# Performance work log

Hardware: AMD Instinct MI355X
Metric: run time of the kernel (lower is better)

## Reference

```python
import jax, jax.numpy as jnp
import numpy as np
import math

B, L, M, D, EL, H = 128, 105, 55, 256, 3, 1
PATCH = [3, 5, 7]

def pos_embed(T, d):
    pos = jnp.arange(T, dtype=jnp.float32)[:, None]
    div = jnp.exp(jnp.arange(0, d, 2, dtype=jnp.float32) * (-math.log(10000.0) / d))
    pe = jnp.zeros((T, d), dtype=jnp.float32)
    pe = pe.at[:, 0::2].set(jnp.sin(pos * div))
    pe = pe.at[:, 1::2].set(jnp.cos(pos * div))
    return pe

def circular_conv(x, w):
    # x: [N, T, Cin], w: [Dout, Cin, 3]; Conv1d kernel 3, circular padding 1, no bias
    xc = jnp.pad(x.transpose(0, 2, 1), ((0, 0), (0, 0), (1, 1)), mode='wrap')
    y = jax.lax.conv_general_dilated(xc, w, (1,), 'VALID', dimension_numbers=('NCH', 'OIH', 'NCH'))
    return y.transpose(0, 2, 1)

def _forward(x, conv_p0, conv_n0, conv_p1, conv_n1, conv_p2, conv_n2, Wq, bq, Wk, bk):
    convs = [(conv_p0, conv_n0), (conv_p1, conv_n1), (conv_p2, conv_n2)]
    # RevIN 'norm': per-sample standardization over time; stats are detached in torch
    mean = jax.lax.stop_gradient(jnp.mean(x, axis=1, keepdims=True))
    std = jax.lax.stop_gradient(jnp.sqrt(jnp.var(x, axis=1, keepdims=True) + 1e-5))
    xr = (x - mean) / std                      # [B, L, M]
    xt = xr.transpose(0, 2, 1)                 # [B, M, L]
    dk = D // H
    scale = 1.0 / math.sqrt(dk)
    series_list, prior_list = [], []
    for i, p in enumerate(PATCH):
        n = L // p
        # patch-size branch: (b m) n p -> embed over n with in_channels=p
        x_size = circular_conv(xt.reshape(B * M, n, p), convs[i][0]) + pos_embed(n, D)
        # patch-num branch: (b m) p n -> embed over p with in_channels=n
        x_num = circular_conv(xt.reshape(B * M, p, n), convs[i][1]) + pos_embed(p, D)
        for l in range(EL):
            def attn_mean(z):
                T = z.shape[1]
                q = (z @ Wq[l] + bq[l]).reshape(B * M, T, H, dk)
                k = (z @ Wk[l] + bk[l]).reshape(B * M, T, H, dk)
                a = jax.nn.softmax(scale * jnp.einsum('blhe,bshe->bhls', q, k), axis=-1)
                # fuse: mean over channel BEFORE expanding to window size
                # (repeat/tile commutes with the channel-mean, avoids [B*M,H,L,L])
                return a.reshape(B, M, H, T, T).mean(axis=1)   # [B, H, T, T]
            a_size = attn_mean(x_size)                          # [B, H, n, n]
            # einops repeat '(m rm) (n rn)': element-wise contiguous repeat
            series_list.append(jnp.repeat(jnp.repeat(a_size, p, axis=-2), p, axis=-1))
            a_num = attn_mean(x_num)                            # [B, H, p, p]
            # torch .repeat: tiling
            prior_list.append(jnp.tile(a_num, (1, 1, n, n)))
    # order: patch-major, layer-minor (matches the flattened lists)
    return jnp.stack(series_list), jnp.stack(prior_list)        # each [9, B, H, L, L]

def setup_inputs():
    key = jax.random.key(0)
    ks = jax.random.split(key, 12)
    s = 0.05
    inp = {"x": jax.random.normal(ks[0], (B, L, M), jnp.float32)}
    for i, p in enumerate(PATCH):
        inp[f"conv_p{i}"] = s * jax.random.normal(ks[1 + 2 * i], (D, p, 3), jnp.float32)
        inp[f"conv_n{i}"] = s * jax.random.normal(ks[2 + 2 * i], (D, L // p, 3), jnp.float32)
    inp["Wq"] = s * jax.random.normal(ks[7], (EL, D, D), jnp.float32)
    inp["bq"] = jnp.zeros((EL, D), jnp.float32)
    inp["Wk"] = s * jax.random.normal(ks[8], (EL, D, D), jnp.float32)
    inp["bk"] = jnp.zeros((EL, D), jnp.float32)
    return inp

def reference(x, conv_p0, conv_n0, conv_p1, conv_n1, conv_p2, conv_n2, Wq, bq, Wk, bk):
    return _forward(x, conv_p0, conv_n0, conv_p1, conv_n1, conv_p2, conv_n2, Wq, bq, Wk, bk)
```

## Files before the change

### kernel.cpp

```cpp
#include <hip/hip_runtime.h>
#include <hip/hip_bf16.h>

#define B_ 128
#define L_ 105
#define M_ 55
#define D_ 256
#define NCOMBO 18

#define WS_XT    0
#define WS_PE    739200
#define WS_LEFT  761216
#define WS_RIGHT 1258880
#define WS_MM    1756544
#define WS_MP    761216
#define WS_ACC   1258880
#define LR_STRIDE 27648
#define MM_STRIDE 11664
#define MP_STRIDE 12544
#define ACC_TOT  758016

#define WS_LRP        1966592
#define LRP_KZ_STRIDE 27648
#define LRP_C_STRIDE  110592
#define LRP_HALF      1990656
#define WS_NEED_BYTES ((size_t)(WS_LRP + 2 * LRP_HALF) * 4)

__constant__ int c_peOff[6] = {0, 35, 38, 59, 64, 79};
__constant__ int c_accbase[18] = {0,1225,2450, 3675,3684,3693, 3702,4143,4584,
                                  5025,5050,5075, 5100,5325,5550, 5775,5824,5873};

__device__ __forceinline__ void combo_dims(int c, int& i, int& br, int& l,
                                           int& p, int& n, int& Cin, int& T, int& J) {
    i = c / 6; br = (c % 6) / 3; l = c % 3;
    p = 3 + 2 * i;
    n = L_ / p;
    Cin = br ? n : p;
    T   = br ? p : n;
    J = 3 * Cin;
}

__device__ __forceinline__ float dot4(float4 a, float4 b) {
    return a.x * b.x + a.y * b.y + a.z * b.z + a.w * b.w;
}

__global__ void revin_kernel(const float* __restrict__ x, float* __restrict__ ws) {
    int bm = blockIdx.x; int b = bm / M_; int m = bm % M_;
    int tid = threadIdx.x;
    __shared__ float s1[128], s2[128];
    float v = 0.f;
    if (tid < L_) v = x[(b * L_ + tid) * M_ + m];
    s1[tid] = v; s2[tid] = v * v;
    __syncthreads();
    for (int off = 64; off > 0; off >>= 1) {
        if (tid < off) { s1[tid] += s1[tid + off]; s2[tid] += s2[tid + off]; }
        __syncthreads();
    }
    float mean = s1[0] * (1.f / L_);
    float var  = s2[0] * (1.f / L_) - mean * mean;
    float rstd = rsqrtf(var + 1e-5f);
    if (tid < L_) ws[WS_XT + bm * L_ + tid] = (v - mean) * rstd;
}

__global__ void pe_kernel(float* __restrict__ ws) {
    int bi = blockIdx.x;
    int i = bi / 2, br = bi % 2;
    int p = 3 + 2 * i, n = L_ / p;
    int T = br ? p : n;
    int d = threadIdx.x;
    float divv = expf(-(float)(d & ~1) * (logf(10000.f) / (float)D_));
    float* base = ws + WS_PE + c_peOff[bi] * D_;
    for (int t = 0; t < T; ++t) {
        float arg = (float)t * divv;
        base[t * D_ + d] = (d & 1) ? cosf(arg) : sinf(arg);
    }
}

__global__ __launch_bounds__(256) void lr2_kernel(
                          const float* __restrict__ w0, const float* __restrict__ w1,
                          const float* __restrict__ w2c, const float* __restrict__ w3,
                          const float* __restrict__ w4, const float* __restrict__ w5,
                          const float* __restrict__ Wq, const float* __restrict__ bq,
                          const float* __restrict__ Wk, const float* __restrict__ bk,
                          float* __restrict__ ws) {
    int c = blockIdx.x;
    int i, br, l, p, n, Cin, T, J; combo_dims(c, i, br, l, p, n, Cin, T, J);
    int Mdim = J + T;
    int r0 = blockIdx.y * 8;
    if (r0 >= Mdim) return;
    int kz = blockIdx.z;
    int d0 = kz * 64;
    int wi = i * 2 + br;
    const float* conv = (wi == 0) ? w0 : (wi == 1) ? w1 : (wi == 2) ? w2c
                       : (wi == 3) ? w3 : (wi == 4) ? w4 : w5;
    __shared__ float S[8][64];
    int tid = threadIdx.x;
    for (int idx = tid; idx < 8 * 64; idx += 256) {
        int rr = idx >> 6, dd = idx & 63;
        int row = r0 + rr; float val = 0.f;
        int d = d0 + dd;
        if (row < J) val = conv[d * J + row];
        else if (row < Mdim) val = ws[WS_PE + (c_peOff[wi] + (row - J)) * D_ + d];
        S[rr][dd] = val;
    }
    __syncthreads();
    const float* wqp = Wq + l * D_ * D_;
    const float* wkp = Wk + l * D_ * D_;
    float accL[8], accR[8];
#pragma unroll
    for (int rr = 0; rr < 8; ++rr) { accL[rr] = 0.f; accR[rr] = 0.f; }
    int o = tid;
#pragma unroll 8
    for (int dd = 0; dd < 64; ++dd) {
        int d = d0 + dd;
        float wqv = wqp[d * D_ + o];
        float wkv = wkp[d * D_ + o];
#pragma unroll
        for (int rr = 0; rr < 8; ++rr) {
            float sv = S[rr][dd];
            accL[rr] += sv * wqv;
            accR[rr] += sv * wkv;
        }
    }
    float bqv = (kz == 0) ? bq[l * D_ + o] : 0.f;
    float bkv = (kz == 0) ? bk[l * D_ + o] : 0.f;
    float* Lp = ws + WS_LRP + c * LRP_C_STRIDE + kz * LRP_KZ_STRIDE;
    float* Rp = Lp + LRP_HALF;
#pragma unroll
    for (int rr = 0; rr < 8; ++rr) {
        int row = r0 + rr;
        if (row < Mdim) {
            float aq = (row >= J) ? bqv : 0.f;
            float ak = (row >= J) ? bkv : 0.f;
            Lp[row * D_ + o] = accL[rr] + aq;
            Rp[row * D_ + o] = accR[rr] + ak;
        }
    }
}

__global__ __launch_bounds__(256) void lr_kernel(
                          const float* __restrict__ w0, const float* __restrict__ w1,
                          const float* __restrict__ w2c, const float* __restrict__ w3,
                          const float* __restrict__ w4, const float* __restrict__ w5,
                          const float* __restrict__ Wq, const float* __restrict__ bq,
                          const float* __restrict__ Wk, const float* __restrict__ bk,
                          float* __restrict__ ws) {
    int c = blockIdx.x;
    int i, br, l, p, n, Cin, T, J; combo_dims(c, i, br, l, p, n, Cin, T, J);
    int Mdim = J + T;
    int r0 = blockIdx.y * 4;
    if (r0 >= Mdim) return;
    int wi = i * 2 + br;
    const float* conv = (wi == 0) ? w0 : (wi == 1) ? w1 : (wi == 2) ? w2c
                       : (wi == 3) ? w3 : (wi == 4) ? w4 : w5;
    __shared__ float S[4][256];
    int tid = threadIdx.x;
    for (int idx = tid; idx < 4 * 256; idx += 256) {
        int rr = idx >> 8, dd = idx & 255;
        int row = r0 + rr; float val = 0.f;
        if (row < J) val = conv[dd * J + row];
        else if (row < Mdim) val = ws[WS_PE + (c_peOff[wi] + (row - J)) * D_ + dd];
        S[rr][dd] = val;
    }
    __syncthreads();
    const float* wqp = Wq + l * D_ * D_;
    const float* wkp = Wk + l * D_ * D_;
    float accL[4], accR[4];
#pragma unroll
    for (int rr = 0; rr < 4; ++rr) { accL[rr] = 0.f; accR[rr] = 0.f; }
    int o = tid;
#pragma unroll 8
    for (int d = 0; d < D_; ++d) {
        float wqv = wqp[d * D_ + o];
        float wkv = wkp[d * D_ + o];
#pragma unroll
        for (int rr = 0; rr < 4; ++rr) {
            float sv = S[rr][d];
            accL[rr] += sv * wqv;
            accR[rr] += sv * wkv;
        }
    }
    float bqv = bq[l * D_ + o], bkv = bk[l * D_ + o];
#pragma unroll
    for (int rr = 0; rr < 4; ++rr) {
        int row = r0 + rr;
        if (row < Mdim) {
            float aq = (row >= J) ? bqv : 0.f;
            float ak = (row >= J) ? bkv : 0.f;
            ws[WS_LEFT  + c * LR_STRIDE + row * D_ + o] = accL[rr] + aq;
            ws[WS_RIGHT + c * LR_STRIDE + row * D_ + o] = accR[rr] + ak;
        }
    }
}

__global__ void mm_kernel(float* __restrict__ ws, int use_partial) {
    int c = blockIdx.x;
    int i, br, l, p, n, Cin, T, J; combo_dims(c, i, br, l, p, n, Cin, T, J);
    int Mdim = J + T;
    int tr = blockIdx.y / 7, tc = blockIdx.y % 7;
    int r0 = tr * 16, c0 = tc * 16;
    if (r0 >= Mdim || c0 >= Mdim) return;
    __shared__ __align__(16) float Lb[16][260], Rb[16][260];
    int tid = threadIdx.x;
    if (use_partial) {
        const float* Lp = ws + WS_LRP + c * LRP_C_STRIDE;
        const float* Rp = Lp + LRP_HALF;
        for (int idx = tid; idx < 16 * 256; idx += 256) {
            int rr = idx >> 8, d = idx & 255;
            int rL = r0 + rr, rR = c0 + rr;
            float lv = 0.f, rv = 0.f;
            if (rL < Mdim) {
                int base = rL * D_ + d;
                lv = Lp[base] + Lp[base + LRP_KZ_STRIDE]
                   + Lp[base + 2 * LRP_KZ_STRIDE] + Lp[base + 3 * LRP_KZ_STRIDE];
            }
            if (rR < Mdim) {
                int base = rR * D_ + d;
                rv = Rp[base] + Rp[base + LRP_KZ_STRIDE]
                   + Rp[base + 2 * LRP_KZ_STRIDE] + Rp[base + 3 * LRP_KZ_STRIDE];
            }
            Lb[rr][d] = lv; Rb[rr][d] = rv;
        }
    } else {
        for (int idx = tid; idx < 16 * 256; idx += 256) {
            int rr = idx >> 8, d = idx & 255;
            int rL = r0 + rr, rR = c0 + rr;
            Lb[rr][d] = (rL < Mdim) ? ws[WS_LEFT  + c * LR_STRIDE + rL * D_ + d] : 0.f;
            Rb[rr][d] = (rR < Mdim) ? ws[WS_RIGHT + c * LR_STRIDE + rR * D_ + d] : 0.f;
        }
    }
    __syncthreads();
    int rr = tid / 16, cc = tid % 16;
    const float4* lrow = (const float4*)(&Lb[rr][0]);
    const float4* rrow = (const float4*)(&Rb[cc][0]);
    float acc = 0.f;
#pragma unroll 8
    for (int d4 = 0; d4 < 64; ++d4) {
        float4 a = lrow[d4], bb = rrow[d4];
        acc += a.x * bb.x + a.y * bb.y + a.z * bb.z + a.w * bb.w;
    }
    int r = r0 + rr, cth = c0 + cc;
    if (r < Mdim && cth < Mdim)
        ws[WS_MM + c * MM_STRIDE + r * Mdim + cth] = acc;
}

__global__ void pack_kernel(float* __restrict__ ws) {
    int c = blockIdx.x;
    int i, br, l, p, n, Cin, T, J; combo_dims(c, i, br, l, p, n, Cin, T, J);
    int Mdim = J + T;
    int Cinp = (Cin + 3) & ~3;
    int Jp = 3 * Cinp;
    int T4 = (T + 3) & ~3;
    int W = Jp + T4;
    const float* MMc = ws + WS_MM + c * MM_STRIDE;
    float* Mp = ws + WS_MP + c * MP_STRIDE;
    for (int e = threadIdx.x; e < W * W; e += 256) {
        int r = e / W, o = e % W;
        int srcr = -1, srcc = -1;
        bool brow = false;
        if (r < Jp) {
            int k = r / Cinp, cin = r % Cinp;
            if (cin < Cin) srcr = cin * 3 + k;
        } else {
            int t = r - Jp;
            if (t < T) { srcr = J + t; brow = true; }
        }
        if (o < Jp) {
            int k2 = o / Cinp, cin2 = o % Cinp;
            if (cin2 < Cin) srcc = cin2 * 3 + k2;
        } else {
            int s = o - Jp;
            if (s < T) srcc = J + s;
        }
        float val;
        if (srcr >= 0 && srcc >= 0) val = MMc[srcr * Mdim + srcc];
        else if (brow && o >= Jp && srcc < 0) val = -1e30f;
        else val = 0.f;
        Mp[e] = val;
    }
}

__global__ void zero_acc(float* __restrict__ ws) {
    int idx = blockIdx.x * 256 + threadIdx.x;
    if (idx < ACC_TOT / 4) {
        float4 z; z.x = 0.f; z.y = 0.f; z.z = 0.f; z.w = 0.f;
        ((float4*)(ws + WS_ACC))[idx] = z;
    }
}

template<int P, int BR>
__global__ __launch_bounds__(256) void attn2(const float* __restrict__ ws,
                                             float* __restrict__ wsw) {
    constexpr int N    = L_ / P;
    constexpr int Cin  = BR ? N : P;
    constexpr int T    = BR ? P : N;
    constexpr int Cinp = (Cin + 3) & ~3;
    constexpr int Jp   = 3 * Cinp;
    constexpr int JP4  = Jp / 4;
    constexpr int T4   = (T + 3) & ~3;
    constexpr int W    = Jp + T4;
    constexpr int W4   = W / 4;
    constexpr int WP4  = W4 + 1;
    constexpr int WP   = WP4 * 4;
    constexpr int ST   = T4 + 1;
    constexpr int II   = (P - 3) / 2;
    constexpr int MC   = BR ? (P == 3 ? 12 : 8) : (P == 7 ? 8 : 4);
    constexpr int TH   = (BR == 0 && P == 3) ? 2 : 1;
    constexpr int TSUB = (T + TH - 1) / TH;
    constexpr int NT   = (MC / 4) * TSUB * W4;
    constexpr int TPB  = (NT + 255) / 256;
    constexpr int MCQ  = MC / 4;
    constexpr int CQ   = Cinp / 4;
    constexpr int CQP  = CQ | 1;
    constexpr int S4N  = T4 / 4;
    constexpr int XTR4 = Cinp * MCQ + 1;

    constexpr int OFF_X2A = 0;
    constexpr int SZ_X2A  = MC * T * CQP * 4;
    constexpr int OFF_G   = OFF_X2A + SZ_X2A;
    constexpr int SZ_G    = MC * TSUB * WP;
    constexpr int OFF_X2T = OFF_G + SZ_G;
    constexpr int SZ_X2T  = T * XTR4 * 4;
    constexpr int OFF_S   = OFF_X2T;
    constexpr int SZ_S    = MC * TSUB * ST;
    constexpr int TOT     = OFF_X2T + ((SZ_X2T > SZ_S) ? SZ_X2T : SZ_S);
    static_assert(TOT * 4 <= 65536, "LDS budget");

    __shared__ __align__(16) float smem[TOT];
    const int tid = threadIdx.x;
    const int b = blockIdx.x, l = blockIdx.y;
    const int sp = blockIdx.z / TH;
    const int th = blockIdx.z % TH;
    const int t0 = th * TSUB;
    const int TC = (T - t0 < TSUB) ? (T - t0) : TSUB;
    const int c = II * 6 + BR * 3 + l;
    const int m0 = sp * MC;
    const int vm = (M_ - m0 < MC) ? (M_ - m0) : MC;

    const float*  Mpg  = ws + WS_MP + c * MP_STRIDE;
    const float4* Mpg4 = (const float4*)Mpg;

    for (int e = tid; e < MC * T * CQP * 4; e += 256) {
        int cin  = e % (CQP * 4);
        int trow = (e / (CQP * 4)) % T;
        int mcol = e / (CQP * 4 * T);
        float v = 0.f;
        if (cin < Cin && m0 + mcol < M_)
            v = ws[WS_XT + (size_t)(b * M_ + m0 + mcol) * L_ + trow * Cin + cin];
        smem[OFF_X2A + e] = v;
    }
    for (int e = tid; e < T * XTR4 * 4; e += 256) {
        int w    = e % (XTR4 * 4);
        int trow = e / (XTR4 * 4);
        float v = 0.f;
        if (w < Cinp * MC) {
            int mcol = w % MC, cin = w / MC;
            if (cin < Cin && m0 + mcol < M_)
                v = ws[WS_XT + (size_t)(b * M_ + m0 + mcol) * L_ + trow * Cin + cin];
        }
        smem[OFF_X2T + e] = v;
    }

    const float4* X2T4 = (const float4*)(smem + OFF_X2T);
    const float4* X2A4 = (const float4*)(smem + OFF_X2A);
    float4*       G4w  = (float4*)(smem + OFF_G);
    const float4* G4   = (const float4*)(smem + OFF_G);

    float a[TPB][4][4];
#pragma unroll
    for (int tt = 0; tt < TPB; ++tt) {
        int q = tid + tt * 256;
        if (q < NT) {
            int o4 = q % W4, tl = (q / W4) % TSUB;
            if (tl < TC) {
                float4 bv = Mpg4[(Jp + t0 + tl) * W4 + o4];
#pragma unroll
                for (int am = 0; am < 4; ++am) {
                    a[tt][am][0] = bv.x; a[tt][am][1] = bv.y;
                    a[tt][am][2] = bv.z; a[tt][am][3] = bv.w;
                }
            }
        }
    }
    __syncthreads();
#pragma unroll
    for (int k = 0; k < 3; ++k) {
#pragma unroll
        for (int tt = 0; tt < TPB; ++tt) {
            int q = tid + tt * 256;
            if (q < NT) {
                int o4 = q % W4, tl = (q / W4) % TSUB, m4 = q / (W4 * TSUB);
                if (tl < TC) {
                    int trow = t0 + tl + k - 1;
                    if (trow < 0) trow += T;
                    if (trow >= T) trow -= T;
                    const float4* xp = X2T4 + trow * XTR4 + m4;
                    const float4* mp = Mpg4 + k * Cinp * W4 + o4;
#pragma unroll 4
                    for (int cin = 0; cin < Cinp; ++cin) {
                        float4 x4 = xp[cin * MCQ];
                        float4 mv = mp[cin * W4];
#pragma unroll
                        for (int aq = 0; aq < 4; ++aq) {
                            float m = (aq == 0) ? mv.x : (aq == 1) ? mv.y
                                    : (aq == 2) ? mv.z : mv.w;
                            a[tt][0][aq] += x4.x * m;
                            a[tt][1][aq] += x4.y * m;
                            a[tt][2][aq] += x4.z * m;
                            a[tt][3][aq] += x4.w * m;
                        }
                    }
                }
            }
        }
    }
#pragma unroll
    for (int tt = 0; tt < TPB; ++tt) {
        int q = tid + tt * 256;
        if (q < NT) {
            int o4 = q % W4, tl = (q / W4) % TSUB, m4 = q / (W4 * TSUB);
            if (tl < TC) {
#pragma unroll
                for (int am = 0; am < 4; ++am) {
                    float4 o;
                    o.x = a[tt][am][0]; o.y = a[tt][am][1];
                    o.z = a[tt][am][2]; o.w = a[tt][am][3];
                    G4w[((m4 * 4 + am) * TSUB + tl) * WP4 + o4] = o;
                }
            }
        }
    }
    __syncthreads();

    for (int it = tid; it < MC * TSUB * S4N; it += 256) {
        int tl = it % TSUB;
        int s4 = (it / TSUB) % S4N;
        int mc = it / (TSUB * S4N);
        if (tl >= TC) continue;
        int grow = (mc * TSUB + tl) * WP4;
        float4 bi = G4[grow + JP4 + s4];
        float acc[4] = {bi.x, bi.y, bi.z, bi.w};
#pragma unroll 2
        for (int cinq = 0; cinq < CQ; ++cinq) {
            float4 xr[6];
#pragma unroll
            for (int kk = 0; kk < 6; ++kk) {
                int r = s4 * 4 - 1 + kk;
                if (r < 0) r += T;
                if (r >= T) r -= T;
                xr[kk] = X2A4[(mc * T + r) * CQP + cinq];
            }
#pragma unroll
            for (int k = 0; k < 3; ++k) {
                float4 g = G4[grow + k * CQ + cinq];
#pragma unroll
                for (int q = 0; q < 4; ++q) {
                    float4 x4 = xr[q + k];
                    acc[q] += g.x * x4.x + g.y * x4.y + g.z * x4.z + g.w * x4.w;
                }
            }
        }
#pragma unroll
        for (int q = 0; q < 4; ++q)
            smem[OFF_S + (mc * TSUB + tl) * ST + s4 * 4 + q] = 0.0625f * acc[q];
    }
    __syncthreads();

    for (int rid = tid; rid < MC * TSUB; rid += 256) {
        int mc = rid / TSUB, tl = rid % TSUB;
        if (tl >= TC) continue;
        int base = OFF_S + (mc * TSUB + tl) * ST;
        float pr[T4];
#pragma unroll
        for (int s = 0; s < T4; ++s) pr[s] = smem[base + s];
        float mx = -1e30f;
#pragma unroll
        for (int s = 0; s < T4; ++s) mx = fmaxf(mx, pr[s]);
        float sum = 0.f;
#pragma unroll
        for (int s = 0; s < T4; ++s) { pr[s] = __expf(pr[s] - mx); sum += pr[s]; }
        float inv = 1.f / sum;
#pragma unroll
        for (int s = 0; s < T; ++s) smem[base + s] = pr[s] * inv;
    }
    __syncthreads();

    float* accp = wsw + WS_ACC + c_accbase[c] * 128 + b * T * T;
    for (int e = tid; e < TC * T; e += 256) {
        int tl = e / T, s = e % T;
        float v = 0.f;
        for (int mc = 0; mc < vm; ++mc)
            v += smem[OFF_S + (mc * TSUB + tl) * ST + s];
        atomicAdd(&accp[(t0 + tl) * T + s], v);
    }
}

template<int P, int BR>
__device__ __forceinline__ void expand_body(const float* __restrict__ acc,
                                            float* __restrict__ outp) {
    constexpr int T = BR ? P : (L_ / P);
    for (int idx = threadIdx.x; idx < L_ * L_; idx += 256) {
        int r = idx / L_, c2 = idx % L_;
        int rt = BR ? (r % P) : (r / P);
        int ct = BR ? (c2 % P) : (c2 / P);
        outp[idx] = acc[rt * T + ct];
    }
}

__global__ __launch_bounds__(256) void expand_kernel(const float* __restrict__ ws,
                                                     float* __restrict__ out) {
    int c = blockIdx.x, b = blockIdx.y;
    int i = c / 6, br = (c % 6) / 3, l = c % 3;
    int p = 3 + 2 * i;
    int T = br ? p : (L_ / p);
    __shared__ float sAcc[1232];
    int abase = c_accbase[c] * 128 + b * T * T;
    for (int idx = threadIdx.x; idx < T * T; idx += 256)
        sAcc[idx] = ws[WS_ACC + abase + idx] * (1.f / (float)M_);
    __syncthreads();
    float* outp = out + ((size_t)(br * 9 + i * 3 + l) * B_ + (size_t)b) * (size_t)(L_ * L_);
    int key = i * 2 + br;
    switch (key) {
        case 0: expand_body<3, 0>(sAcc, outp); break;
        case 1: expand_body<3, 1>(sAcc, outp); break;
        case 2: expand_body<5, 0>(sAcc, outp); break;
        case 3: expand_body<5, 1>(sAcc, outp); break;
        case 4: expand_body<7, 0>(sAcc, outp); break;
        case 5: expand_body<7, 1>(sAcc, outp); break;
    }
}

extern "C" void kernel_launch(void* const* d_in, const int* in_sizes, int n_in,
                              void* d_out, int out_size, void* d_ws, size_t ws_size,
                              hipStream_t stream) {
    const float* x   = (const float*)d_in[0];
    const float* cp0 = (const float*)d_in[1];
    const float* cn0 = (const float*)d_in[2];
    const float* cp1 = (const float*)d_in[3];
    const float* cn1 = (const float*)d_in[4];
    const float* cp2 = (const float*)d_in[5];
    const float* cn2 = (const float*)d_in[6];
    const float* Wq  = (const float*)d_in[7];
    const float* bq  = (const float*)d_in[8];
    const float* Wk  = (const float*)d_in[9];
    const float* bk  = (const float*)d_in[10];
    float* ws = (float*)d_ws;
    float* out = (float*)d_out;

    const int use_partial = (ws_size >= WS_NEED_BYTES) ? 1 : 0;

    hipLaunchKernelGGL(revin_kernel, dim3(B_ * M_), dim3(128), 0, stream, x, ws);
    hipLaunchKernelGGL(pe_kernel, dim3(6), dim3(256), 0, stream, ws);
    if (use_partial) {
        hipLaunchKernelGGL(lr2_kernel, dim3(NCOMBO, 14, 4), dim3(256), 0, stream,
                           cp0, cn0, cp1, cn1, cp2, cn2, Wq, bq, Wk, bk, ws);
    } else {
        hipLaunchKernelGGL(lr_kernel, dim3(NCOMBO, 27), dim3(256), 0, stream,
                           cp0, cn0, cp1, cn1, cp2, cn2, Wq, bq, Wk, bk, ws);
    }
    hipLaunchKernelGGL(mm_kernel, dim3(NCOMBO, 49), dim3(256), 0, stream, ws, use_partial);
    hipLaunchKernelGGL(pack_kernel, dim3(NCOMBO), dim3(256), 0, stream, ws);
    hipLaunchKernelGGL(zero_acc, dim3((ACC_TOT / 4 + 255) / 256), dim3(256), 0, stream, ws);

    hipLaunchKernelGGL((attn2<3, 0>), dim3(B_, 3, 28), dim3(256), 0, stream, ws, ws);
    hipLaunchKernelGGL((attn2<3, 1>), dim3(B_, 3, 5),  dim3(256), 0, stream, ws, ws);
    hipLaunchKernelGGL((attn2<5, 0>), dim3(B_, 3, 14), dim3(256), 0, stream, ws, ws);
    hipLaunchKernelGGL((attn2<5, 1>), dim3(B_, 3, 7),  dim3(256), 0, stream, ws, ws);
    hipLaunchKernelGGL((attn2<7, 0>), dim3(B_, 3, 7),  dim3(256), 0, stream, ws, ws);
    hipLaunchKernelGGL((attn2<7, 1>), dim3(B_, 3, 7),  dim3(256), 0, stream, ws, ws);

    hipLaunchKernelGGL(expand_kernel, dim3(NCOMBO, B_), dim3(256), 0, stream, ws, out);
}
```

Measured before the change: 476.0 us.

## Loop encoder layers inside attn2 blocks and stage weight slices in LDS

The three encoder layers move from a grid dimension into a loop inside each attention block. The block now loads its input tiles (X2A, X2T) into LDS once and reuses them across all three layers instead of reloading them per layer. Each k-slice of the projected weight matrix is also copied into a new LDS region before the inner product, rather than being read from global memory. In exchange the grid has a third as many blocks, which lowers parallelism, and each layer step adds more __syncthreads barriers.

```diff
diff --git a/kernel.cpp b/kernel.cpp
--- a/kernel.cpp
+++ b/kernel.cpp
@@ -320,24 +320,25 @@
     constexpr int SZ_G    = MC * TSUB * WP;
     constexpr int OFF_X2T = OFF_G + SZ_G;
     constexpr int SZ_X2T  = T * XTR4 * 4;
-    constexpr int OFF_S   = OFF_X2T;
+    constexpr int OFF_MS  = OFF_X2T + SZ_X2T;
+    constexpr int SZ_MSL  = Cinp * W;
     constexpr int SZ_S    = MC * TSUB * ST;
-    constexpr int TOT     = OFF_X2T + ((SZ_X2T > SZ_S) ? SZ_X2T : SZ_S);
+    constexpr int SZ_MS   = (SZ_MSL > SZ_S) ? SZ_MSL : SZ_S;
+    constexpr int OFF_MSL = OFF_MS;
+    constexpr int OFF_S   = OFF_MS;
+    constexpr int TOT     = OFF_MS + SZ_MS;
     static_assert(TOT * 4 <= 65536, "LDS budget");
 
     __shared__ __align__(16) float smem[TOT];
     const int tid = threadIdx.x;
-    const int b = blockIdx.x, l = blockIdx.y;
-    const int sp = blockIdx.z / TH;
-    const int th = blockIdx.z % TH;
+    const int b = blockIdx.x;
+    const int zz = blockIdx.y;
+    const int sp = zz / TH;
+    const int th = zz % TH;
     const int t0 = th * TSUB;
     const int TC = (T - t0 < TSUB) ? (T - t0) : TSUB;
-    const int c = II * 6 + BR * 3 + l;
     const int m0 = sp * MC;
     const int vm = (M_ - m0 < MC) ? (M_ - m0) : MC;
-
-    const float*  Mpg  = ws + WS_MP + c * MP_STRIDE;
-    const float4* Mpg4 = (const float4*)Mpg;
 
     for (int e = tid; e < MC * T * CQP * 4; e += 256) {
         int cin  = e % (CQP * 4);
@@ -359,138 +360,149 @@
         }
         smem[OFF_X2T + e] = v;
     }
+    __syncthreads();
 
     const float4* X2T4 = (const float4*)(smem + OFF_X2T);
     const float4* X2A4 = (const float4*)(smem + OFF_X2A);
+    float4*       MSL4 = (float4*)(smem + OFF_MSL);
     float4*       G4w  = (float4*)(smem + OFF_G);
     const float4* G4   = (const float4*)(smem + OFF_G);
 
-    float a[TPB][4][4];
-#pragma unroll
-    for (int tt = 0; tt < TPB; ++tt) {
-        int q = tid + tt * 256;
-        if (q < NT) {
-            int o4 = q % W4, tl = (q / W4) % TSUB;
-            if (tl < TC) {
-                float4 bv = Mpg4[(Jp + t0 + tl) * W4 + o4];
-#pragma unroll
-                for (int am = 0; am < 4; ++am) {
-                    a[tt][am][0] = bv.x; a[tt][am][1] = bv.y;
-                    a[tt][am][2] = bv.z; a[tt][am][3] = bv.w;
+    for (int l = 0; l < 3; ++l) {
+        const int c = II * 6 + BR * 3 + l;
+        const float*  Mpg  = ws + WS_MP + c * MP_STRIDE;
+        const float4* Mpg4 = (const float4*)Mpg;
+
+        float a[TPB][4][4];
+#pragma unroll
+        for (int tt = 0; tt < TPB; ++tt) {
+            int q = tid + tt * 256;
+            if (q < NT) {
+                int o4 = q % W4, tl = (q / W4) % TSUB;
+                if (tl < TC) {
+                    float4 bv = Mpg4[(Jp + t0 + tl) * W4 + o4];
+#pragma unroll
+                    for (int am = 0; am < 4; ++am) {
+                        a[tt][am][0] = bv.x; a[tt][am][1] = bv.y;
+                        a[tt][am][2] = bv.z; a[tt][am][3] = bv.w;
+                    }
                 }
             }
         }
-    }
-    __syncthreads();
-#pragma unroll
-    for (int k = 0; k < 3; ++k) {
+        for (int k = 0; k < 3; ++k) {
+            for (int e = tid; e < Cinp * W4; e += 256)
+                MSL4[e] = Mpg4[k * Cinp * W4 + e];
+            __syncthreads();
+#pragma unroll
+            for (int tt = 0; tt < TPB; ++tt) {
+                int q = tid + tt * 256;
+                if (q < NT) {
+                    int o4 = q % W4, tl = (q / W4) % TSUB, m4 = q / (W4 * TSUB);
+                    if (tl < TC) {
+                        int trow = t0 + tl + k - 1;
+                        if (trow < 0) trow += T;
+                        if (trow >= T) trow -= T;
+                        const float4* xp = X2T4 + trow * XTR4 + m4;
+                        const float4* mp = MSL4 + o4;
+#pragma unroll 4
+                        for (int cin = 0; cin < Cinp; ++cin) {
+                            float4 x4 = xp[cin * MCQ];
+                            float4 mv = mp[cin * W4];
+#pragma unroll
+                            for (int aq = 0; aq < 4; ++aq) {
+                                float m = (aq == 0) ? mv.x : (aq == 1) ? mv.y
+                                        : (aq == 2) ? mv.z : mv.w;
+                                a[tt][0][aq] += x4.x * m;
+                                a[tt][1][aq] += x4.y * m;
+                                a[tt][2][aq] += x4.z * m;
+                                a[tt][3][aq] += x4.w * m;
+                            }
+                        }
+                    }
+                }
+            }
+            __syncthreads();
+        }
 #pragma unroll
         for (int tt = 0; tt < TPB; ++tt) {
             int q = tid + tt * 256;
             if (q < NT) {
                 int o4 = q % W4, tl = (q / W4) % TSUB, m4 = q / (W4 * TSUB);
                 if (tl < TC) {
-                    int trow = t0 + tl + k - 1;
-                    if (trow < 0) trow += T;
-                    if (trow >= T) trow -= T;
-                    const float4* xp = X2T4 + trow * XTR4 + m4;
-                    const float4* mp = Mpg4 + k * Cinp * W4 + o4;
-#pragma unroll 4
-                    for (int cin = 0; cin < Cinp; ++cin) {
-                        float4 x4 = xp[cin * MCQ];
-                        float4 mv = mp[cin * W4];
-#pragma unroll
-                        for (int aq = 0; aq < 4; ++aq) {
-                            float m = (aq == 0) ? mv.x : (aq == 1) ? mv.y
-                                    : (aq == 2) ? mv.z : mv.w;
-                            a[tt][0][aq] += x4.x * m;
-                            a[tt][1][aq] += x4.y * m;
-                            a[tt][2][aq] += x4.z * m;
-                            a[tt][3][aq] += x4.w * m;
-                        }
+#pragma unroll
+                    for (int am = 0; am < 4; ++am) {
+                        float4 o;
+                        o.x = a[tt][am][0]; o.y = a[tt][am][1];
+                        o.z = a[tt][am][2]; o.w = a[tt][am][3];
+                        G4w[((m4 * 4 + am) * TSUB + tl) * WP4 + o4] = o;
                     }
                 }
             }
         }
-    }
-#pragma unroll
-    for (int tt = 0; tt < TPB; ++tt) {
-        int q = tid + tt * 256;
-        if (q < NT) {
-            int o4 = q % W4, tl = (q / W4) % TSUB, m4 = q / (W4 * TSUB);
-            if (tl < TC) {
-#pragma unroll
-                for (int am = 0; am < 4; ++am) {
-                    float4 o;
-                    o.x = a[tt][am][0]; o.y = a[tt][am][1];
-                    o.z = a[tt][am][2]; o.w = a[tt][am][3];
-                    G4w[((m4 * 4 + am) * TSUB + tl) * WP4 + o4] = o;
+        __syncthreads();
+
+        for (int it = tid; it < MC * TSUB * S4N; it += 256) {
+            int tl = it % TSUB;
+            int s4 = (it / TSUB) % S4N;
+            int mc = it / (TSUB * S4N);
+            if (tl >= TC) continue;
+            int grow = (mc * TSUB + tl) * WP4;
+            float4 bi = G4[grow + JP4 + s4];
+            float acc[4] = {bi.x, bi.y, bi.z, bi.w};
+#pragma unroll 2
+            for (int cinq = 0; cinq < CQ; ++cinq) {
+                float4 xr[6];
+#pragma unroll
+                for (int kk = 0; kk < 6; ++kk) {
+                    int r = s4 * 4 - 1 + kk;
+                    if (r < 0) r += T;
+                    if (r >= T) r -= T;
+                    xr[kk] = X2A4[(mc * T + r) * CQP + cinq];
+                }
+#pragma unroll
+                for (int k = 0; k < 3; ++k) {
+                    float4 g = G4[grow + k * CQ + cinq];
+#pragma unroll
+                    for (int q = 0; q < 4; ++q) {
+                        float4 x4 = xr[q + k];
+                        acc[q] += g.x * x4.x + g.y * x4.y + g.z * x4.z + g.w * x4.w;
+                    }
                 }
             }
-        }
-    }
-    __syncthreads();
-
-    for (int it = tid; it < MC * TSUB * S4N; it += 256) {
-        int tl = it % TSUB;
-        int s4 = (it / TSUB) % S4N;
-        int mc = it / (TSUB * S4N);
-        if (tl >= TC) continue;
-        int grow = (mc * TSUB + tl) * WP4;
-        float4 bi = G4[grow + JP4 + s4];
-        float acc[4] = {bi.x, bi.y, bi.z, bi.w};
-#pragma unroll 2
-        for (int cinq = 0; cinq < CQ; ++cinq) {
-            float4 xr[6];
-#pragma unroll
-            for (int kk = 0; kk < 6; ++kk) {
-                int r = s4 * 4 - 1 + kk;
-                if (r < 0) r += T;
-                if (r >= T) r -= T;
-                xr[kk] = X2A4[(mc * T + r) * CQP + cinq];
-            }
-#pragma unroll
-            for (int k = 0; k < 3; ++k) {
-                float4 g = G4[grow + k * CQ + cinq];
-#pragma unroll
-                for (int q = 0; q < 4; ++q) {
-                    float4 x4 = xr[q + k];
-                    acc[q] += g.x * x4.x + g.y * x4.y + g.z * x4.z + g.w * x4.w;
-                }
-            }
-        }
-#pragma unroll
-        for (int q = 0; q < 4; ++q)
-            smem[OFF_S + (mc * TSUB + tl) * ST + s4 * 4 + q] = 0.0625f * acc[q];
-    }
-    __syncthreads();
-
-    for (int rid = tid; rid < MC * TSUB; rid += 256) {
-        int mc = rid / TSUB, tl = rid % TSUB;
-        if (tl >= TC) continue;
-        int base = OFF_S + (mc * TSUB + tl) * ST;
-        float pr[T4];
-#pragma unroll
-        for (int s = 0; s < T4; ++s) pr[s] = smem[base + s];
-        float mx = -1e30f;
-#pragma unroll
-        for (int s = 0; s < T4; ++s) mx = fmaxf(mx, pr[s]);
-        float sum = 0.f;
-#pragma unroll
-        for (int s = 0; s < T4; ++s) { pr[s] = __expf(pr[s] - mx); sum += pr[s]; }
-        float inv = 1.f / sum;
-#pragma unroll
-        for (int s = 0; s < T; ++s) smem[base + s] = pr[s] * inv;
-    }
-    __syncthreads();
-
-    float* accp = wsw + WS_ACC + c_accbase[c] * 128 + b * T * T;
-    for (int e = tid; e < TC * T; e += 256) {
-        int tl = e / T, s = e % T;
-        float v = 0.f;
-        for (int mc = 0; mc < vm; ++mc)
-            v += smem[OFF_S + (mc * TSUB + tl) * ST + s];
-        atomicAdd(&accp[(t0 + tl) * T + s], v);
+#pragma unroll
+            for (int q = 0; q < 4; ++q)
+                smem[OFF_S + (mc * TSUB + tl) * ST + s4 * 4 + q] = 0.0625f * acc[q];
+        }
+        __syncthreads();
+
+        for (int rid = tid; rid < MC * TSUB; rid += 256) {
+            int mc = rid / TSUB, tl = rid % TSUB;
+            if (tl >= TC) continue;
+            int base = OFF_S + (mc * TSUB + tl) * ST;
+            float pr[T4];
+#pragma unroll
+            for (int s = 0; s < T4; ++s) pr[s] = smem[base + s];
+            float mx = -1e30f;
+#pragma unroll
+            for (int s = 0; s < T4; ++s) mx = fmaxf(mx, pr[s]);
+            float sum = 0.f;
+#pragma unroll
+            for (int s = 0; s < T4; ++s) { pr[s] = __expf(pr[s] - mx); sum += pr[s]; }
+            float inv = 1.f / sum;
+#pragma unroll
+            for (int s = 0; s < T; ++s) smem[base + s] = pr[s] * inv;
+        }
+        __syncthreads();
+
+        float* accp = wsw + WS_ACC + c_accbase[c] * 128 + b * T * T;
+        for (int e = tid; e < TC * T; e += 256) {
+            int tl = e / T, s = e % T;
+            float v = 0.f;
+            for (int mc = 0; mc < vm; ++mc)
+                v += smem[OFF_S + (mc * TSUB + tl) * ST + s];
+            atomicAdd(&accp[(t0 + tl) * T + s], v);
+        }
+        __syncthreads();
     }
 }
 
@@ -561,12 +573,12 @@
     hipLaunchKernelGGL(pack_kernel, dim3(NCOMBO), dim3(256), 0, stream, ws);
     hipLaunchKernelGGL(zero_acc, dim3((ACC_TOT / 4 + 255) / 256), dim3(256), 0, stream, ws);
 
-    hipLaunchKernelGGL((attn2<3, 0>), dim3(B_, 3, 28), dim3(256), 0, stream, ws, ws);
-    hipLaunchKernelGGL((attn2<3, 1>), dim3(B_, 3, 5),  dim3(256), 0, stream, ws, ws);
-    hipLaunchKernelGGL((attn2<5, 0>), dim3(B_, 3, 14), dim3(256), 0, stream, ws, ws);
-    hipLaunchKernelGGL((attn2<5, 1>), dim3(B_, 3, 7),  dim3(256), 0, stream, ws, ws);
-    hipLaunchKernelGGL((attn2<7, 0>), dim3(B_, 3, 7),  dim3(256), 0, stream, ws, ws);
-    hipLaunchKernelGGL((attn2<7, 1>), dim3(B_, 3, 7),  dim3(256), 0, stream, ws, ws);
+    hipLaunchKernelGGL((attn2<3, 0>), dim3(B_, 28), dim3(256), 0, stream, ws, ws);
+    hipLaunchKernelGGL((attn2<3, 1>), dim3(B_, 5),  dim3(256), 0, stream, ws, ws);
+    hipLaunchKernelGGL((attn2<5, 0>), dim3(B_, 14), dim3(256), 0, stream, ws, ws);
+    hipLaunchKernelGGL((attn2<5, 1>), dim3(B_, 7),  dim3(256), 0, stream, ws, ws);
+    hipLaunchKernelGGL((attn2<7, 0>), dim3(B_, 7),  dim3(256), 0, stream, ws, ws);
+    hipLaunchKernelGGL((attn2<7, 1>), dim3(B_, 7),  dim3(256), 0, stream, ws, ws);
 
     hipLaunchKernelGGL(expand_kernel, dim3(NCOMBO, B_), dim3(256), 0, stream, ws, out);
 }
```

Result: slower. 490.2 us (+3.0%).
